# Kernel optimization log

Hardware: AMD Instinct MI355X
Metric: run time of the kernel (lower is better)

The kernel has to match this reference:

```python
import jax, jax.numpy as jnp
import numpy as np

BN_EPS = 1e-5

SOBEL_X = jnp.array([[-1., 0., 1.], [-2., 0., 2.], [-1., 0., 1.]], jnp.float32).reshape(1, 1, 3, 3)
SOBEL_Y = jnp.array([[-1., -2., -1.], [0., 0., 0.], [1., 2., 1.]], jnp.float32).reshape(1, 1, 3, 3)


def _conv2d(x, w, stride, pad):
    return jax.lax.conv_general_dilated(x, w, window_strides=(stride, stride),
                                        padding=((pad, pad), (pad, pad)),
                                        dimension_numbers=('NCHW', 'OIHW', 'NCHW'))


def _resize_bilinear_align_corners(x, H, W):
    # x: [b,c,h1,w1] -> [b,c,H,W], align_corners=True
    b, c, h1, w1 = x.shape
    ys = jnp.linspace(0., h1 - 1., H)
    xs = jnp.linspace(0., w1 - 1., W)
    y0 = jnp.floor(ys).astype(jnp.int32)
    x0 = jnp.floor(xs).astype(jnp.int32)
    y1 = jnp.minimum(y0 + 1, h1 - 1)
    x1 = jnp.minimum(x0 + 1, w1 - 1)
    wy = (ys - y0)[None, None, :, None]
    wx = (xs - x0)[None, None, None, :]
    top = x[:, :, y0, :]
    bot = x[:, :, y1, :]
    top = top[:, :, :, x0] * (1. - wx) + top[:, :, :, x1] * wx
    bot = bot[:, :, :, x0] * (1. - wx) + bot[:, :, :, x1] * wx
    return top * (1. - wy) + bot * wy


def setup_inputs() -> dict:
    key = jax.random.key(0)
    ks = jax.random.split(key, 6)
    b, c, h, w = 4, 64, 128, 128
    return {
        'x': jax.random.normal(ks[0], (b, c, h, w), jnp.float32),
        'conv_w': jax.random.normal(ks[1], (c, c, 3, 3), jnp.float32) * 0.05,
        'conv_b': jax.random.normal(ks[2], (c,), jnp.float32) * 0.05,
        'bn_gamma': jnp.ones((c,), jnp.float32),
        'bn_beta': jnp.zeros((c,), jnp.float32),
        'bn_mean': jnp.zeros((c,), jnp.float32),
        'bn_var': jnp.ones((c,), jnp.float32),
        'fc1_w': jax.random.normal(ks[3], (c, c), jnp.float32) * 0.1,
        'fc2_w': jax.random.normal(ks[4], (c, c), jnp.float32) * 0.1,
        'fc3_w': jax.random.normal(ks[5], (c, c), jnp.float32) * 0.1,
    }


def reference(x, conv_w, conv_b, bn_gamma, bn_beta, bn_mean, bn_var, fc1_w, fc2_w, fc3_w):
    b, c, h, w = x.shape
    # input block: conv s2 + BN (eval) + relu
    y = _conv2d(x, conv_w, 2, 1) + conv_b[None, :, None, None]
    y = (y - bn_mean[None, :, None, None]) * jax.lax.rsqrt(bn_var + BN_EPS)[None, :, None, None]
    y = jax.nn.relu(y * bn_gamma[None, :, None, None] + bn_beta[None, :, None, None])
    b, c, h1, w1 = y.shape
    N = h1 * w1
    # pre: [b,c,h1,w1] -> [b,1,N,c]
    xp = y.reshape(b, c, N).transpose(0, 2, 1).reshape(b, 1, N, c)
    # Sobel adjacency over the N "node" axis
    sx = jnp.abs(_conv2d(xp, SOBEL_X, 1, 1)).reshape(b, N, c)
    sy = jnp.abs(_conv2d(xp, SOBEL_Y, 1, 1)).reshape(b, N, c)
    A = jnp.einsum('bnc,bmc->bnm', sx, sy)  # [b,N,N]
    # torch nn.Softmax() (no dim) on a 3D tensor => legacy dim=0 (batch axis)
    A = jax.nn.softmax(A, axis=0)
    # normalize: D^-0.5 (A + I) D^-0.5, batched
    A1 = A + jnp.eye(N, dtype=A.dtype)[None]
    dinv = A1.sum(axis=2) ** -0.5  # [b,N]
    A = dinv[:, :, None] * A1 * dinv[:, None, :]
    # GCN propagation; Conv1d k=1 no-bias == channel matmul
    xg = xp.reshape(b, N, c)
    xg = jax.nn.relu(jnp.einsum('bnm,bmc,oc->bno', A, xg, fc1_w))
    xg = jax.nn.relu(jnp.einsum('bnm,bmc,oc->bno', A, xg, fc2_w))
    xg = jnp.einsum('bnm,bmc,oc->bon', A, xg, fc3_w)  # [b,c,N]
    out = xg.reshape(b, c, h1, w1)
    return _resize_bilinear_align_corners(out, h, w)
```

## Files before the change

### kernel.cpp

```cpp
#include <hip/hip_runtime.h>
#include <hip/hip_bf16.h>

typedef float f32x4 __attribute__((ext_vector_type(4)));
typedef short bf16x8 __attribute__((ext_vector_type(8)));

#define NB 4
#define NC 64
#define NH 128
#define NW 128
#define NN 4096
#define BN_EPS_C 1e-5f

__device__ __forceinline__ void gld16(const void* g, void* l) {
    __builtin_amdgcn_global_load_lds((const __attribute__((address_space(1))) void*)g,
                                     (__attribute__((address_space(3))) void*)l, 16, 0, 0);
}
__device__ __forceinline__ unsigned pk2(float a, float b) {
    __hip_bfloat16 x = __float2bfloat16(a), y = __float2bfloat16(b);
    return (unsigned)*(unsigned short*)&x | ((unsigned)*(unsigned short*)&y << 16);
}

__global__ __launch_bounds__(256) void k_wrep(const float* __restrict__ cw, float* __restrict__ W3)
{
    int idx = blockIdx.x * 256 + threadIdx.x;
    if (idx >= 16 * 64 * 36) return;
    int oq = idx / (64 * 36);
    int rem = idx - oq * (64 * 36);
    int ic = rem / 36;
    int j = rem - ic * 36;
    int oc4 = j / 9, kk = j - oc4 * 9;
    W3[((size_t)oq * 64 + ic) * 48 + oc4 * 12 + kk] = cw[(((size_t)(oq * 4 + oc4)) * 64 + ic) * 9 + kk];
}

__global__ __launch_bounds__(256) void k_conv(
    const float* __restrict__ x, const float* __restrict__ W3, const float* __restrict__ cb,
    const float* __restrict__ bng, const float* __restrict__ bnb, const float* __restrict__ bnm,
    const float* __restrict__ bnv, float* __restrict__ xg)
{
    int oh = blockIdx.x, quad = blockIdx.y, b = blockIdx.z;
    int tid = threadIdx.x;
    int ow = tid & 63;
    int w = __builtin_amdgcn_readfirstlane(tid >> 6);
    int ocg = quad * 4 + w;
    float acc[4] = {0.f, 0.f, 0.f, 0.f};
    const float* xb = x + (size_t)b * NC * NH * NW;
    const float* wbase = W3 + (size_t)ocg * 64 * 48;
    int ih0 = 2 * oh - 1;
    for (int ic = 0; ic < 64; ++ic) {
        const float* xr = xb + (size_t)ic * (NH * NW);
        float v00, v01, v02, v10, v11, v12, v20, v21, v22;
        if (ih0 < 0) { v00 = v01 = v02 = 0.f; }
        else {
            const float* p = xr + ih0 * NW + 2 * ow;
            float2 t = *(const float2*)p;
            v01 = t.x; v02 = t.y;
            v00 = (ow == 0) ? 0.f : p[-1];
        }
        { const float* p = xr + (ih0 + 1) * NW + 2 * ow; float2 t = *(const float2*)p; v11 = t.x; v12 = t.y; v10 = (ow == 0) ? 0.f : p[-1]; }
        { const float* p = xr + (ih0 + 2) * NW + 2 * ow; float2 t = *(const float2*)p; v21 = t.x; v22 = t.y; v20 = (ow == 0) ? 0.f : p[-1]; }
        const float* wp = wbase + ic * 48;
#pragma unroll
        for (int j = 0; j < 4; ++j) {
            const float* wj = wp + j * 12;
            acc[j] += wj[0] * v00 + wj[1] * v01 + wj[2] * v02
                    + wj[3] * v10 + wj[4] * v11 + wj[5] * v12
                    + wj[6] * v20 + wj[7] * v21 + wj[8] * v22;
        }
    }
    int n = oh * 64 + ow;
    int oc0 = ocg * 4;
    f32x4 r;
#pragma unroll
    for (int j = 0; j < 4; ++j) {
        int oc = oc0 + j;
        float s = bng[oc] * rsqrtf(bnv[oc] + BN_EPS_C);
        float y = (acc[j] + cb[oc] - bnm[oc]) * s + bnb[oc];
        r[j] = fmaxf(y, 0.f);
    }
    *(f32x4*)(xg + ((size_t)b * NN + n) * 64 + oc0) = r;
}

__global__ __launch_bounds__(256) void k_sobel(
    const float* __restrict__ xg,
    __hip_bfloat16* __restrict__ xh, __hip_bfloat16* __restrict__ xl,
    __hip_bfloat16* __restrict__ yh, __hip_bfloat16* __restrict__ yl)
{
    __shared__ float t[66][66];
    int b = blockIdx.y;
    int n0 = blockIdx.x * 64;
    int tid = threadIdx.x;
    const float* xb = xg + (size_t)b * NN * 64;
    for (int idx = tid; idx < 66 * 64; idx += 256) {
        int r = idx >> 6, c = idx & 63;
        int n = n0 - 1 + r;
        float v = (n >= 0 && n < NN) ? xb[(size_t)n * 64 + c] : 0.f;
        t[r][c + 1] = v;
    }
    for (int idx = tid; idx < 66; idx += 256) { t[idx][0] = 0.f; t[idx][65] = 0.f; }
    __syncthreads();
    int c = tid & 63, rg = tid >> 6;
    int lc = c + 1;
    for (int i = 0; i < 16; ++i) {
        int r = rg * 16 + i;
        float tm1 = t[r][lc - 1],     t0 = t[r][lc],     tp1 = t[r][lc + 1];
        float mm1 = t[r + 1][lc - 1],                    mp1 = t[r + 1][lc + 1];
        float bm1 = t[r + 2][lc - 1], b0 = t[r + 2][lc], bp1 = t[r + 2][lc + 1];
        float gx = (tp1 + 2.f * mp1 + bp1) - (tm1 + 2.f * mm1 + bm1);
        float gy = (bm1 + 2.f * b0 + bp1) - (tm1 + 2.f * t0 + tp1);
        float ax = fabsf(gx), ay = fabsf(gy);
        size_t o = ((size_t)b * NN + n0 + r) * 64 + c;
        __hip_bfloat16 h1 = __float2bfloat16(ax);
        xh[o] = h1;
        xl[o] = __float2bfloat16(ax - __bfloat162float(h1));
        __hip_bfloat16 h2 = __float2bfloat16(ay);
        yh[o] = h2;
        yl[o] = __float2bfloat16(ay - __bfloat162float(h2));
    }
}

__global__ __launch_bounds__(256, 2) void k_logits(
    const __hip_bfloat16* __restrict__ xh_, const __hip_bfloat16* __restrict__ xl_,
    const __hip_bfloat16* __restrict__ yh_, const __hip_bfloat16* __restrict__ yl_,
    __hip_bfloat16* __restrict__ A, float* __restrict__ rowsum)
{
    __shared__ __align__(16) ushort xs[2][2][4096];
    const ushort* xh = (const ushort*)xh_;
    const ushort* xl = (const ushort*)xl_;
    const ushort* yh = (const ushort*)yh_;
    const ushort* yl = (const ushort*)yl_;
    int tid = threadIdx.x, lane = tid & 63;
    int wv = __builtin_amdgcn_readfirstlane(tid >> 6);
    int l15 = lane & 15, lg = lane >> 4;
    int m0 = blockIdx.x * 128, n0 = blockIdx.y * 64;

    f32x4 acc[4][2][4];
#pragma unroll
    for (int b = 0; b < 4; ++b)
#pragma unroll
        for (int t = 0; t < 2; ++t)
#pragma unroll
            for (int u = 0; u < 4; ++u) acc[b][t][u] = (f32x4){0.f, 0.f, 0.f, 0.f};

#define STAGEX(buf, b_) do { \
    _Pragma("unroll") \
    for (int p = 0; p < 2; ++p) { \
        int ch = p * 256 + tid; \
        int r = ch >> 3; \
        int sc = ((ch & 7) ^ (r & 7)) * 8; \
        gld16(xh + ((size_t)(b_) * NN + n0 + r) * 64 + sc, (char*)xs[buf][0] + ch * 16); \
        gld16(xl + ((size_t)(b_) * NN + n0 + r) * 64 + sc, (char*)xs[buf][1] + ch * 16); \
    } \
} while (0)

#define YLOAD(Y, b_) do { \
    _Pragma("unroll") \
    for (int t = 0; t < 2; ++t) { \
        size_t rb = ((size_t)(b_) * NN + m0 + wv * 32 + t * 16 + l15) * 64 + lg * 8; \
        Y[t][0][0] = *(const bf16x8*)(yh + rb); \
        Y[t][1][0] = *(const bf16x8*)(yh + rb + 32); \
        Y[t][0][1] = *(const bf16x8*)(yl + rb); \
        Y[t][1][1] = *(const bf16x8*)(yl + rb + 32); \
    } \
} while (0)

#define COMPUTE(buf, Y, b_) do { \
    _Pragma("unroll") \
    for (int ks = 0; ks < 2; ++ks) { \
        bf16x8 xf[4][2]; \
        _Pragma("unroll") \
        for (int u = 0; u < 4; ++u) { \
            int r = u * 16 + l15; \
            int c16 = (ks * 4 + lg) ^ (r & 7); \
            xf[u][0] = *(const bf16x8*)((const char*)xs[buf][0] + r * 128 + c16 * 16); \
            xf[u][1] = *(const bf16x8*)((const char*)xs[buf][1] + r * 128 + c16 * 16); \
        } \
        _Pragma("unroll") \
        for (int t = 0; t < 2; ++t) \
            _Pragma("unroll") \
            for (int u = 0; u < 4; ++u) { \
                f32x4 a = acc[b_][t][u]; \
                a = __builtin_amdgcn_mfma_f32_16x16x32_bf16(Y[t][ks][0], xf[u][0], a, 0, 0, 0); \
                a = __builtin_amdgcn_mfma_f32_16x16x32_bf16(Y[t][ks][0], xf[u][1], a, 0, 0, 0); \
                a = __builtin_amdgcn_mfma_f32_16x16x32_bf16(Y[t][ks][1], xf[u][0], a, 0, 0, 0); \
                acc[b_][t][u] = a; \
            } \
    } \
} while (0)

    bf16x8 yA[2][2][2], yB[2][2][2];
    STAGEX(0, 0); YLOAD(yA, 0);
    __syncthreads();
    STAGEX(1, 1); YLOAD(yB, 1); COMPUTE(0, yA, 0);
    __syncthreads();
    STAGEX(0, 2); YLOAD(yA, 2); COMPUTE(1, yB, 1);
    __syncthreads();
    STAGEX(1, 3); YLOAD(yB, 3); COMPUTE(0, yA, 2);
    __syncthreads();
    COMPUTE(1, yB, 3);
#undef STAGEX
#undef YLOAD
#undef COMPUTE

    float rsum[4][4];
#pragma unroll
    for (int b = 0; b < 4; ++b)
#pragma unroll
        for (int u = 0; u < 4; ++u) rsum[b][u] = 0.f;

#pragma unroll
    for (int t = 0; t < 2; ++t)
#pragma unroll
        for (int u = 0; u < 4; ++u) {
            float av[4][4];
#pragma unroll
            for (int j = 0; j < 4; ++j) {
                float v0 = acc[0][t][u][j], v1 = acc[1][t][u][j];
                float v2 = acc[2][t][u][j], v3 = acc[3][t][u][j];
                float mx = fmaxf(fmaxf(v0, v1), fmaxf(v2, v3));
                float e0 = __expf(v0 - mx), e1 = __expf(v1 - mx);
                float e2 = __expf(v2 - mx), e3 = __expf(v3 - mx);
                float rz = 1.f / (e0 + e1 + e2 + e3);
                av[0][j] = e0 * rz; av[1][j] = e1 * rz;
                av[2][j] = e2 * rz; av[3][j] = e3 * rz;
                rsum[0][u] += av[0][j]; rsum[1][u] += av[1][j];
                rsum[2][u] += av[2][j]; rsum[3][u] += av[3][j];
            }
            int n = n0 + u * 16 + l15;
            int m = m0 + wv * 32 + t * 16 + lg * 4;
#pragma unroll
            for (int b = 0; b < 4; ++b) {
                uint2 pv;
                pv.x = pk2(av[b][0], av[b][1]);
                pv.y = pk2(av[b][2], av[b][3]);
                *(uint2*)((ushort*)A + (size_t)b * NN * NN + (size_t)n * NN + m) = pv;
            }
        }

#pragma unroll
    for (int b = 0; b < 4; ++b)
#pragma unroll
        for (int u = 0; u < 4; ++u) {
            float s = rsum[b][u];
            s += __shfl_xor(s, 16);
            s += __shfl_xor(s, 32);
            if (lane < 16)
                atomicAdd(&rowsum[(size_t)b * NN + n0 + u * 16 + l15], s);
        }
}

__global__ __launch_bounds__(256) void k_dinv(const float* __restrict__ rs, float* __restrict__ dinv)
{
    int i = blockIdx.x * 256 + threadIdx.x;
    dinv[i] = rsqrtf(rs[i] + 1.0f);
}

__global__ __launch_bounds__(256) void k_small(
    const float* __restrict__ h, const float* __restrict__ fc, const float* __restrict__ dinv,
    __hip_bfloat16* __restrict__ tT, float* __restrict__ tf)
{
    int blk = blockIdx.x;
    int b = blk >> 6, m0 = (blk & 63) * 64;
    int tid = threadIdx.x;
    int mi = tid & 63, m = m0 + mi;
    int oq = __builtin_amdgcn_readfirstlane(tid >> 6);
    const float* hr = h + ((size_t)b * NN + m) * 64;
    float hv[64];
#pragma unroll
    for (int i = 0; i < 16; ++i) {
        float4 v = *(const float4*)(hr + 4 * i);
        hv[4 * i] = v.x; hv[4 * i + 1] = v.y; hv[4 * i + 2] = v.z; hv[4 * i + 3] = v.w;
    }
    float dv = dinv[(size_t)b * NN + m];
#pragma unroll
    for (int j = 0; j < 16; ++j) {
        int o = oq * 16 + j;
        const float* wr = fc + (size_t)o * 64;
        float a = 0.f;
#pragma unroll
        for (int c2 = 0; c2 < 64; ++c2) a += hv[c2] * wr[c2];
        a *= dv;
        tf[((size_t)b * NN + m) * 64 + o] = a;
        tT[((size_t)b * 64 + o) * NN + m] = __float2bfloat16(a);
    }
}

__global__ __launch_bounds__(256) void k_big(
    const __hip_bfloat16* __restrict__ A_, const __hip_bfloat16* __restrict__ tT_,
    float* __restrict__ part)
{
    __shared__ __align__(16) ushort ab[2][4096];
    const ushort* A = (const ushort*)A_;
    const ushort* tT = (const ushort*)tT_;
    int blk = blockIdx.x;
    int ntile = blk & 63, b = (blk >> 6) & 3, ks = blk >> 8;
    int n0 = ntile * 64;
    int tid = threadIdx.x, lane = tid & 63;
    int w = __builtin_amdgcn_readfirstlane(tid >> 6);
    int l15 = lane & 15, lg = lane >> 4;
    size_t kw0 = (size_t)ks * 1024;
    const ushort* Ab = A + (size_t)b * NN * NN;
    const ushort* Tb = tT + ((size_t)b * 64 + w * 16 + l15) * NN + kw0;

    f32x4 acc[4];
#pragma unroll
    for (int ti = 0; ti < 4; ++ti) acc[ti] = (f32x4){0.f, 0.f, 0.f, 0.f};

#define STAGE(buf, s) do { \
    _Pragma("unroll") \
    for (int p = 0; p < 2; ++p) { \
        int ch = p * 256 + tid; \
        int r = ch >> 3; \
        int sc = ((ch & 7) ^ (r & 7)) * 8; \
        gld16(Ab + (size_t)(n0 + r) * NN + kw0 + (size_t)(s) * 64 + sc, (char*)ab[buf] + ch * 16); \
    } \
} while (0)

    STAGE(0, 0);
    bf16x8 bf0 = *(const bf16x8*)(Tb + lg * 8);
    bf16x8 bf1 = *(const bf16x8*)(Tb + 32 + lg * 8);
    bf16x8 nf0 = bf0, nf1 = bf1;
    __syncthreads();

    int cur = 0;
    for (int s = 0; s < 16; ++s) {
        if (s < 15) {
            STAGE(cur ^ 1, s + 1);
            nf0 = *(const bf16x8*)(Tb + (size_t)(s + 1) * 64 + lg * 8);
            nf1 = *(const bf16x8*)(Tb + (size_t)(s + 1) * 64 + 32 + lg * 8);
        }
#pragma unroll
        for (int kc = 0; kc < 2; ++kc) {
            bf16x8 bfr = (kc == 0) ? bf0 : bf1;
#pragma unroll
            for (int ti = 0; ti < 4; ++ti) {
                int r = ti * 16 + l15;
                int c16 = (kc * 4 + lg) ^ (r & 7);
                bf16x8 afr = *(const bf16x8*)((const char*)ab[cur] + r * 128 + c16 * 16);
                acc[ti] = __builtin_amdgcn_mfma_f32_16x16x32_bf16(afr, bfr, acc[ti], 0, 0, 0);
            }
        }
        bf0 = nf0; bf1 = nf1;
        __syncthreads();
        cur ^= 1;
    }
#undef STAGE

    float* pp = part + ((size_t)(ks * 4 + b) * NN + n0) * 64;
#pragma unroll
    for (int ti = 0; ti < 4; ++ti)
#pragma unroll
        for (int j = 0; j < 4; ++j)
            pp[(size_t)(ti * 16 + lg * 4 + j) * 64 + w * 16 + l15] = acc[ti][j];
}

__global__ __launch_bounds__(256) void k_red(
    const float* __restrict__ part, const float* __restrict__ tf, const float* __restrict__ dinv,
    float* __restrict__ outp, int relu)
{
    int v = blockIdx.x * 256 + threadIdx.x;
    size_t e0 = (size_t)v * 4;
    int b = (int)(e0 >> 18);
    int n = (int)((e0 >> 6) & (NN - 1));
    f32x4 u = (f32x4){0.f, 0.f, 0.f, 0.f};
#pragma unroll
    for (int s = 0; s < 4; ++s)
        u += *(const f32x4*)(part + (size_t)s * (4 * (size_t)NN * 64) + e0);
    f32x4 t = *(const f32x4*)(tf + e0);
    float dn = dinv[(size_t)b * NN + n];
    f32x4 r;
#pragma unroll
    for (int j = 0; j < 4; ++j) {
        float vv = dn * (u[j] + t[j]);
        if (relu) vv = fmaxf(vv, 0.f);
        r[j] = vv;
    }
    *(f32x4*)(outp + e0) = r;
}

__global__ __launch_bounds__(256) void k_up(const float* __restrict__ o3, float* __restrict__ outp)
{
    int b = blockIdx.y, Y = blockIdx.x;
    int tid = threadIdx.x;
    int X = tid & 127, cg = tid >> 7;
    int iy = Y * 63; int y0 = iy / 127; float wy = (float)(iy - y0 * 127) * (1.f / 127.f);
    int y1 = min(y0 + 1, 63);
    int ix = X * 63; int x0 = ix / 127; float wx = (float)(ix - x0 * 127) * (1.f / 127.f);
    int x1 = min(x0 + 1, 63);
    const float* p00 = o3 + ((size_t)b * NN + y0 * 64 + x0) * 64;
    const float* p01 = o3 + ((size_t)b * NN + y0 * 64 + x1) * 64;
    const float* p10 = o3 + ((size_t)b * NN + y1 * 64 + x0) * 64;
    const float* p11 = o3 + ((size_t)b * NN + y1 * 64 + x1) * 64;
    float w00 = (1.f - wy) * (1.f - wx), w01 = (1.f - wy) * wx;
    float w10 = wy * (1.f - wx), w11 = wy * wx;
#pragma unroll
    for (int j = 0; j < 32; ++j) {
        int ch = cg * 32 + j;
        float v = w00 * p00[ch] + w01 * p01[ch] + w10 * p10[ch] + w11 * p11[ch];
        outp[(((size_t)b * 64 + ch) * 128 + Y) * 128 + X] = v;
    }
}

extern "C" void kernel_launch(void* const* d_in, const int* in_sizes, int n_in,
                              void* d_out, int out_size, void* d_ws, size_t ws_size,
                              hipStream_t stream)
{
    const float* x   = (const float*)d_in[0];
    const float* cw  = (const float*)d_in[1];
    const float* cb  = (const float*)d_in[2];
    const float* bng = (const float*)d_in[3];
    const float* bnb = (const float*)d_in[4];
    const float* bnm = (const float*)d_in[5];
    const float* bnv = (const float*)d_in[6];
    const float* fc1 = (const float*)d_in[7];
    const float* fc2 = (const float*)d_in[8];
    const float* fc3 = (const float*)d_in[9];
    float* outp = (float*)d_out;

    char* ws = (char*)d_ws;
    size_t off = 0;
    auto alloc = [&](size_t bytes) -> void* {
        void* p = ws + off;
        off += (bytes + 255) & ~(size_t)255;
        return p;
    };
    __hip_bfloat16* Abuf = (__hip_bfloat16*)alloc((size_t)NB * NN * NN * 2);
    float* part   = (float*)alloc((size_t)4 * NB * NN * 64 * 4);
    float* xg     = (float*)alloc((size_t)NB * NN * 64 * 4);
    __hip_bfloat16* sxh = (__hip_bfloat16*)alloc((size_t)NB * NN * 64 * 2);
    __hip_bfloat16* sxl = (__hip_bfloat16*)alloc((size_t)NB * NN * 64 * 2);
    __hip_bfloat16* syh = (__hip_bfloat16*)alloc((size_t)NB * NN * 64 * 2);
    __hip_bfloat16* syl = (__hip_bfloat16*)alloc((size_t)NB * NN * 64 * 2);
    __hip_bfloat16* tT = (__hip_bfloat16*)alloc((size_t)NB * 64 * NN * 2);
    float* tf     = (float*)alloc((size_t)NB * NN * 64 * 4);
    float* h1     = (float*)alloc((size_t)NB * NN * 64 * 4);
    float* h2     = (float*)alloc((size_t)NB * NN * 64 * 4);
    float* o3     = (float*)alloc((size_t)NB * NN * 64 * 4);
    float* rowsum = (float*)alloc((size_t)NB * NN * 4);
    float* dinvb  = (float*)alloc((size_t)NB * NN * 4);
    float* W3     = (float*)alloc((size_t)16 * 64 * 48 * 4);

    hipMemsetAsync(rowsum, 0, (size_t)NB * NN * 4, stream);

    k_wrep<<<144, 256, 0, stream>>>(cw, W3);
    k_conv<<<dim3(64, 4, 4), 256, 0, stream>>>(x, W3, cb, bng, bnb, bnm, bnv, xg);
    k_sobel<<<dim3(64, 4), 256, 0, stream>>>(xg, sxh, sxl, syh, syl);
    k_logits<<<dim3(32, 64), 256, 0, stream>>>(sxh, sxl, syh, syl, Abuf, rowsum);
    k_dinv<<<64, 256, 0, stream>>>(rowsum, dinvb);

    k_small<<<256, 256, 0, stream>>>(xg, fc1, dinvb, tT, tf);
    k_big<<<1024, 256, 0, stream>>>(Abuf, tT, part);
    k_red<<<1024, 256, 0, stream>>>(part, tf, dinvb, h1, 1);

    k_small<<<256, 256, 0, stream>>>(h1, fc2, dinvb, tT, tf);
    k_big<<<1024, 256, 0, stream>>>(Abuf, tT, part);
    k_red<<<1024, 256, 0, stream>>>(part, tf, dinvb, h2, 1);

    k_small<<<256, 256, 0, stream>>>(h2, fc3, dinvb, tT, tf);
    k_big<<<1024, 256, 0, stream>>>(Abuf, tT, part);
    k_red<<<1024, 256, 0, stream>>>(part, tf, dinvb, o3, 0);

    k_up<<<dim3(128, 4), 256, 0, stream>>>(o3, outp);
}
```

Measured before the change: 388.6 us.

## Widen logits blocks to 512 threads and drop LDS staging in A·T GEMM

k_logits now runs 8 waves per block, each computing one 16-row tile instead of two, which halves per-thread accumulators and is meant to raise occupancy. Row sums are first reduced across waves in shared memory, so each block issues one atomic per row instead of one per wave. k_big drops its LDS double buffer and barriers and loads A and T fragments straight into registers with a two-stage register ping-pong. The risk is less coalesced direct global reads of A and higher register pressure under the new launch bounds.

```diff
diff --git a/kernel.cpp b/kernel.cpp
--- a/kernel.cpp
+++ b/kernel.cpp
@@ -118,7 +118,7 @@
     }
 }
 
-__global__ __launch_bounds__(256, 2) void k_logits(
+__global__ __launch_bounds__(512, 4) void k_logits(
     const __hip_bfloat16* __restrict__ xh_, const __hip_bfloat16* __restrict__ xl_,
     const __hip_bfloat16* __restrict__ yh_, const __hip_bfloat16* __restrict__ yl_,
     __hip_bfloat16* __restrict__ A, float* __restrict__ rowsum)
@@ -133,34 +133,26 @@
     int l15 = lane & 15, lg = lane >> 4;
     int m0 = blockIdx.x * 128, n0 = blockIdx.y * 64;
 
-    f32x4 acc[4][2][4];
+    f32x4 acc[4][4];
 #pragma unroll
     for (int b = 0; b < 4; ++b)
 #pragma unroll
-        for (int t = 0; t < 2; ++t)
-#pragma unroll
-            for (int u = 0; u < 4; ++u) acc[b][t][u] = (f32x4){0.f, 0.f, 0.f, 0.f};
+        for (int u = 0; u < 4; ++u) acc[b][u] = (f32x4){0.f, 0.f, 0.f, 0.f};
 
 #define STAGEX(buf, b_) do { \
-    _Pragma("unroll") \
-    for (int p = 0; p < 2; ++p) { \
-        int ch = p * 256 + tid; \
-        int r = ch >> 3; \
-        int sc = ((ch & 7) ^ (r & 7)) * 8; \
-        gld16(xh + ((size_t)(b_) * NN + n0 + r) * 64 + sc, (char*)xs[buf][0] + ch * 16); \
-        gld16(xl + ((size_t)(b_) * NN + n0 + r) * 64 + sc, (char*)xs[buf][1] + ch * 16); \
-    } \
+    int ch = tid; \
+    int r = ch >> 3; \
+    int sc = ((ch & 7) ^ (r & 7)) * 8; \
+    gld16(xh + ((size_t)(b_) * NN + n0 + r) * 64 + sc, (char*)xs[buf][0] + ch * 16); \
+    gld16(xl + ((size_t)(b_) * NN + n0 + r) * 64 + sc, (char*)xs[buf][1] + ch * 16); \
 } while (0)
 
 #define YLOAD(Y, b_) do { \
-    _Pragma("unroll") \
-    for (int t = 0; t < 2; ++t) { \
-        size_t rb = ((size_t)(b_) * NN + m0 + wv * 32 + t * 16 + l15) * 64 + lg * 8; \
-        Y[t][0][0] = *(const bf16x8*)(yh + rb); \
-        Y[t][1][0] = *(const bf16x8*)(yh + rb + 32); \
-        Y[t][0][1] = *(const bf16x8*)(yl + rb); \
-        Y[t][1][1] = *(const bf16x8*)(yl + rb + 32); \
-    } \
+    size_t rb = ((size_t)(b_) * NN + m0 + wv * 16 + l15) * 64 + lg * 8; \
+    Y[0][0] = *(const bf16x8*)(yh + rb); \
+    Y[1][0] = *(const bf16x8*)(yh + rb + 32); \
+    Y[0][1] = *(const bf16x8*)(yl + rb); \
+    Y[1][1] = *(const bf16x8*)(yl + rb + 32); \
 } while (0)
 
 #define COMPUTE(buf, Y, b_) do { \
@@ -175,19 +167,17 @@
             xf[u][1] = *(const bf16x8*)((const char*)xs[buf][1] + r * 128 + c16 * 16); \
         } \
         _Pragma("unroll") \
-        for (int t = 0; t < 2; ++t) \
-            _Pragma("unroll") \
-            for (int u = 0; u < 4; ++u) { \
-                f32x4 a = acc[b_][t][u]; \
-                a = __builtin_amdgcn_mfma_f32_16x16x32_bf16(Y[t][ks][0], xf[u][0], a, 0, 0, 0); \
-                a = __builtin_amdgcn_mfma_f32_16x16x32_bf16(Y[t][ks][0], xf[u][1], a, 0, 0, 0); \
-                a = __builtin_amdgcn_mfma_f32_16x16x32_bf16(Y[t][ks][1], xf[u][0], a, 0, 0, 0); \
-                acc[b_][t][u] = a; \
-            } \
+        for (int u = 0; u < 4; ++u) { \
+            f32x4 a = acc[b_][u]; \
+            a = __builtin_amdgcn_mfma_f32_16x16x32_bf16(Y[ks][0], xf[u][0], a, 0, 0, 0); \
+            a = __builtin_amdgcn_mfma_f32_16x16x32_bf16(Y[ks][0], xf[u][1], a, 0, 0, 0); \
+            a = __builtin_amdgcn_mfma_f32_16x16x32_bf16(Y[ks][1], xf[u][0], a, 0, 0, 0); \
+            acc[b_][u] = a; \
+        } \
     } \
 } while (0)
 
-    bf16x8 yA[2][2][2], yB[2][2][2];
+    bf16x8 yA[2][2], yB[2][2];
     STAGEX(0, 0); YLOAD(yA, 0);
     __syncthreads();
     STAGEX(1, 1); YLOAD(yB, 1); COMPUTE(0, yA, 0);
@@ -208,34 +198,34 @@
         for (int u = 0; u < 4; ++u) rsum[b][u] = 0.f;
 
 #pragma unroll
-    for (int t = 0; t < 2; ++t)
-#pragma unroll
-        for (int u = 0; u < 4; ++u) {
-            float av[4][4];
-#pragma unroll
-            for (int j = 0; j < 4; ++j) {
-                float v0 = acc[0][t][u][j], v1 = acc[1][t][u][j];
-                float v2 = acc[2][t][u][j], v3 = acc[3][t][u][j];
-                float mx = fmaxf(fmaxf(v0, v1), fmaxf(v2, v3));
-                float e0 = __expf(v0 - mx), e1 = __expf(v1 - mx);
-                float e2 = __expf(v2 - mx), e3 = __expf(v3 - mx);
-                float rz = 1.f / (e0 + e1 + e2 + e3);
-                av[0][j] = e0 * rz; av[1][j] = e1 * rz;
-                av[2][j] = e2 * rz; av[3][j] = e3 * rz;
-                rsum[0][u] += av[0][j]; rsum[1][u] += av[1][j];
-                rsum[2][u] += av[2][j]; rsum[3][u] += av[3][j];
-            }
-            int n = n0 + u * 16 + l15;
-            int m = m0 + wv * 32 + t * 16 + lg * 4;
-#pragma unroll
-            for (int b = 0; b < 4; ++b) {
-                uint2 pv;
-                pv.x = pk2(av[b][0], av[b][1]);
-                pv.y = pk2(av[b][2], av[b][3]);
-                *(uint2*)((ushort*)A + (size_t)b * NN * NN + (size_t)n * NN + m) = pv;
-            }
+    for (int u = 0; u < 4; ++u) {
+        float av[4][4];
+#pragma unroll
+        for (int j = 0; j < 4; ++j) {
+            float v0 = acc[0][u][j], v1 = acc[1][u][j];
+            float v2 = acc[2][u][j], v3 = acc[3][u][j];
+            float mx = fmaxf(fmaxf(v0, v1), fmaxf(v2, v3));
+            float e0 = __expf(v0 - mx), e1 = __expf(v1 - mx);
+            float e2 = __expf(v2 - mx), e3 = __expf(v3 - mx);
+            float rz = 1.f / (e0 + e1 + e2 + e3);
+            av[0][j] = e0 * rz; av[1][j] = e1 * rz;
+            av[2][j] = e2 * rz; av[3][j] = e3 * rz;
+            rsum[0][u] += av[0][j]; rsum[1][u] += av[1][j];
+            rsum[2][u] += av[2][j]; rsum[3][u] += av[3][j];
         }
-
+        int n = n0 + u * 16 + l15;
+        int m = m0 + wv * 16 + lg * 4;
+#pragma unroll
+        for (int b = 0; b < 4; ++b) {
+            uint2 pv;
+            pv.x = pk2(av[b][0], av[b][1]);
+            pv.y = pk2(av[b][2], av[b][3]);
+            *(uint2*)((ushort*)A + (size_t)b * NN * NN + (size_t)n * NN + m) = pv;
+        }
+    }
+
+    __syncthreads();
+    float* rl = (float*)xs;
 #pragma unroll
     for (int b = 0; b < 4; ++b)
 #pragma unroll
@@ -243,9 +233,16 @@
             float s = rsum[b][u];
             s += __shfl_xor(s, 16);
             s += __shfl_xor(s, 32);
-            if (lane < 16)
-                atomicAdd(&rowsum[(size_t)b * NN + n0 + u * 16 + l15], s);
+            if (lane < 16) rl[((wv * 4) + b) * 64 + u * 16 + lane] = s;
         }
+    __syncthreads();
+    if (tid < 256) {
+        int b = tid >> 6, n = tid & 63;
+        float s = 0.f;
+#pragma unroll
+        for (int w2 = 0; w2 < 8; ++w2) s += rl[(w2 * 4 + b) * 64 + n];
+        atomicAdd(&rowsum[(size_t)b * NN + n0 + n], s);
+    }
 }
 
 __global__ __launch_bounds__(256) void k_dinv(const float* __restrict__ rs, float* __restrict__ dinv)
@@ -284,11 +281,10 @@
     }
 }
 
-__global__ __launch_bounds__(256) void k_big(
+__global__ __launch_bounds__(256, 4) void k_big(
     const __hip_bfloat16* __restrict__ A_, const __hip_bfloat16* __restrict__ tT_,
     float* __restrict__ part)
 {
-    __shared__ __align__(16) ushort ab[2][4096];
     const ushort* A = (const ushort*)A_;
     const ushort* tT = (const ushort*)tT_;
     int blk = blockIdx.x;
@@ -298,52 +294,42 @@
     int w = __builtin_amdgcn_readfirstlane(tid >> 6);
     int l15 = lane & 15, lg = lane >> 4;
     size_t kw0 = (size_t)ks * 1024;
-    const ushort* Ab = A + (size_t)b * NN * NN;
-    const ushort* Tb = tT + ((size_t)b * 64 + w * 16 + l15) * NN + kw0;
+    const ushort* Ar = A + (size_t)b * NN * NN + (size_t)(n0 + l15) * NN + kw0 + lg * 8;
+    const ushort* Tb = tT + ((size_t)b * 64 + w * 16 + l15) * NN + kw0 + lg * 8;
 
     f32x4 acc[4];
 #pragma unroll
     for (int ti = 0; ti < 4; ++ti) acc[ti] = (f32x4){0.f, 0.f, 0.f, 0.f};
 
-#define STAGE(buf, s) do { \
+    bf16x8 a0[4][2], a1[4][2], b0[2], b1[2];
+
+#define LOADF(aa, bb, s_) do { \
     _Pragma("unroll") \
-    for (int p = 0; p < 2; ++p) { \
-        int ch = p * 256 + tid; \
-        int r = ch >> 3; \
-        int sc = ((ch & 7) ^ (r & 7)) * 8; \
-        gld16(Ab + (size_t)(n0 + r) * NN + kw0 + (size_t)(s) * 64 + sc, (char*)ab[buf] + ch * 16); \
-    } \
+    for (int ti = 0; ti < 4; ++ti) \
+        _Pragma("unroll") \
+        for (int kc = 0; kc < 2; ++kc) \
+            (aa)[ti][kc] = *(const bf16x8*)(Ar + (size_t)ti * 16 * NN + (s_) * 64 + kc * 32); \
+    _Pragma("unroll") \
+    for (int kc = 0; kc < 2; ++kc) \
+        (bb)[kc] = *(const bf16x8*)(Tb + (size_t)(s_) * 64 + kc * 32); \
 } while (0)
-
-    STAGE(0, 0);
-    bf16x8 bf0 = *(const bf16x8*)(Tb + lg * 8);
-    bf16x8 bf1 = *(const bf16x8*)(Tb + 32 + lg * 8);
-    bf16x8 nf0 = bf0, nf1 = bf1;
-    __syncthreads();
-
-    int cur = 0;
-    for (int s = 0; s < 16; ++s) {
-        if (s < 15) {
-            STAGE(cur ^ 1, s + 1);
-            nf0 = *(const bf16x8*)(Tb + (size_t)(s + 1) * 64 + lg * 8);
-            nf1 = *(const bf16x8*)(Tb + (size_t)(s + 1) * 64 + 32 + lg * 8);
-        }
-#pragma unroll
-        for (int kc = 0; kc < 2; ++kc) {
-            bf16x8 bfr = (kc == 0) ? bf0 : bf1;
-#pragma unroll
-            for (int ti = 0; ti < 4; ++ti) {
-                int r = ti * 16 + l15;
-                int c16 = (kc * 4 + lg) ^ (r & 7);
-                bf16x8 afr = *(const bf16x8*)((const char*)ab[cur] + r * 128 + c16 * 16);
-                acc[ti] = __builtin_amdgcn_mfma_f32_16x16x32_bf16(afr, bfr, acc[ti], 0, 0, 0);
-            }
-        }
-        bf0 = nf0; bf1 = nf1;
-        __syncthreads();
-        cur ^= 1;
-    }
-#undef STAGE
+#define MF(aa, bb) do { \
+    _Pragma("unroll") \
+    for (int kc = 0; kc < 2; ++kc) \
+        _Pragma("unroll") \
+        for (int ti = 0; ti < 4; ++ti) \
+            acc[ti] = __builtin_amdgcn_mfma_f32_16x16x32_bf16((aa)[ti][kc], (bb)[kc], acc[ti], 0, 0, 0); \
+} while (0)
+
+    LOADF(a0, b0, 0);
+    for (int s = 0; s < 16; s += 2) {
+        if (s + 1 < 16) LOADF(a1, b1, s + 1);
+        MF(a0, b0);
+        if (s + 2 < 16) LOADF(a0, b0, s + 2);
+        MF(a1, b1);
+    }
+#undef LOADF
+#undef MF
 
     float* pp = part + ((size_t)(ks * 4 + b) * NN + n0) * 64;
 #pragma unroll
@@ -444,7 +430,7 @@
     k_wrep<<<144, 256, 0, stream>>>(cw, W3);
     k_conv<<<dim3(64, 4, 4), 256, 0, stream>>>(x, W3, cb, bng, bnb, bnm, bnv, xg);
     k_sobel<<<dim3(64, 4), 256, 0, stream>>>(xg, sxh, sxl, syh, syl);
-    k_logits<<<dim3(32, 64), 256, 0, stream>>>(sxh, sxl, syh, syl, Abuf, rowsum);
+    k_logits<<<dim3(32, 64), 512, 0, stream>>>(sxh, sxl, syh, syl, Abuf, rowsum);
     k_dinv<<<64, 256, 0, stream>>>(rowsum, dinvb);
 
     k_small<<<256, 256, 0, stream>>>(xg, fc1, dinvb, tT, tf);
```

Result: slower. 516.5 us (+32.9%).
